# Performance work log

Hardware: AMD Instinct MI355X
Metric: run time of the kernel (lower is better)

## Reference

```python
import jax, jax.numpy as jnp
import numpy as np

INPUT_SIZE = 1024
HIDDEN_SIZE = 1024
BATCH = 8192


def setup_inputs() -> dict:
    key = jax.random.key(0)
    ks = jax.random.split(key, 10)
    s_in = 1.0 / np.sqrt(INPUT_SIZE)
    s_h = 1.0 / np.sqrt(HIDDEN_SIZE)
    return {
        "input": jax.random.normal(ks[0], (BATCH, INPUT_SIZE), jnp.float32),
        "hx": jax.random.normal(ks[1], (BATCH, HIDDEN_SIZE), jnp.float32),
        # weights stored [in, out] (transpose of torch Linear)
        "W_ih": jax.random.uniform(ks[2], (INPUT_SIZE, 2 * HIDDEN_SIZE), jnp.float32, -s_in, s_in),
        "b_ih": jax.random.uniform(ks[3], (2 * HIDDEN_SIZE,), jnp.float32, -s_in, s_in),
        "W_hh": jax.random.uniform(ks[4], (HIDDEN_SIZE, 2 * HIDDEN_SIZE), jnp.float32, -s_h, s_h),
        "b_hh": jax.random.uniform(ks[5], (2 * HIDDEN_SIZE,), jnp.float32, -s_h, s_h),
        "W_c": jax.random.uniform(ks[6], (INPUT_SIZE, HIDDEN_SIZE), jnp.float32, -s_in, s_in),
        "b_c": jax.random.uniform(ks[7], (HIDDEN_SIZE,), jnp.float32, -s_in, s_in),
        "W_hc": jax.random.uniform(ks[8], (HIDDEN_SIZE, HIDDEN_SIZE), jnp.float32, -s_h, s_h),
        "b_hc": jax.random.uniform(ks[9], (HIDDEN_SIZE,), jnp.float32, -s_h, s_h),
    }


def reference(input, hx, W_ih, b_ih, W_hh, b_hh, W_c, b_c, W_hc, b_hc):
    H = hx.shape[1]
    gates = jax.nn.sigmoid(input @ W_ih + b_ih + hx @ W_hh + b_hh)  # [B, 2H]
    z_t, r_t = gates[:, :H], gates[:, H:]
    candidate = jnp.tanh(input @ W_c + b_c + r_t * (hx @ W_hc + b_hc))
    return (1.0 - z_t) * hx + z_t * candidate
```

## Files before the change

### kernel.cpp

```cpp
#include <hip/hip_runtime.h>
#include <hip/hip_bf16.h>
#include <cmath>


typedef __attribute__((ext_vector_type(8))) short bf16x8;
typedef __attribute__((ext_vector_type(4))) float f32x4;
typedef unsigned int u32;

typedef const __attribute__((address_space(1))) u32 gu32;
typedef __attribute__((address_space(3))) u32 su32;

__device__ __forceinline__ unsigned short f2bf(float f) {
  union { float f; u32 u; } v; v.f = f;
  u32 u = v.u;
  u += 0x7FFFu + ((u >> 16) & 1u);
  return (unsigned short)(u >> 16);
}
__device__ __forceinline__ void gload16(void* ldsp, const void* gp) {
  __builtin_amdgcn_global_load_lds((gu32*)gp, (su32*)ldsp, 16, 0, 0);
}
__device__ __forceinline__ float sigmf(float x) { return 1.0f / (1.0f + __expf(-x)); }

__global__ __launch_bounds__(256) void cvt_all(
    const float* __restrict__ In, const float* __restrict__ Hx,
    const float* __restrict__ Wih, const float* __restrict__ Whh,
    const float* __restrict__ Wc,  const float* __restrict__ Whc,
    unsigned short* __restrict__ wsIn, unsigned short* __restrict__ wsHx,
    unsigned short* __restrict__ wsWih, unsigned short* __restrict__ wsWhh,
    unsigned short* __restrict__ wsWc,  unsigned short* __restrict__ wsWhc)
{
  int bid = blockIdx.x;
  if (bid < 8192) {
    int gid = bid * 256 + threadIdx.x;
    const float* src; unsigned short* dst; int idx;
    if (gid < (1 << 20)) { src = In; dst = wsIn; idx = gid; }
    else                 { src = Hx; dst = wsHx; idx = gid - (1 << 20); }
    int m = idx >> 7, t = idx & 127;
    const float4* s = (const float4*)(src + (size_t)m * 1024 + t * 8);
    float4 a = s[0], b = s[1];
    int row = m & 127;
    size_t tile = (size_t)(m >> 7) * 32 + (t >> 2);
    int sw = (t & 3) ^ ((row >> 1) & 3);
    bf16x8 v;
    v[0] = (short)f2bf(a.x); v[1] = (short)f2bf(a.y); v[2] = (short)f2bf(a.z); v[3] = (short)f2bf(a.w);
    v[4] = (short)f2bf(b.x); v[5] = (short)f2bf(b.y); v[6] = (short)f2bf(b.z); v[7] = (short)f2bf(b.w);
    *(bf16x8*)(dst + tile * 4096 + row * 32 + sw * 8) = v;
  } else {
    int wb = bid - 8192;
    const float* W; unsigned short* dst; int NW; int local;
    if (wb < 1024)      { W = Wih; dst = wsWih; NW = 2048; local = wb; }
    else if (wb < 2048) { W = Whh; dst = wsWhh; NW = 2048; local = wb - 1024; }
    else if (wb < 2560) { W = Wc;  dst = wsWc;  NW = 1024; local = wb - 2048; }
    else                { W = Whc; dst = wsWhc; NW = 1024; local = wb - 2560; }
    int nb = local >> 5, kb = local & 31;
    int n  = nb * 64 + (threadIdx.x & 63);
    int k0 = kb * 32 + (threadIdx.x >> 6) * 8;
    bf16x8 v;
    #pragma unroll
    for (int b = 0; b < 8; ++b) v[b] = (short)f2bf(W[(size_t)(k0 + b) * NW + n]);
    int row = n & 63;
    size_t tile = (size_t)(n >> 6) * 32 + (k0 >> 5);
    int sw = ((k0 >> 3) & 3) ^ ((row >> 1) & 3);
    *(bf16x8*)(dst + tile * 2048 + row * 32 + sw * 8) = v;
  }
}

__global__ __launch_bounds__(256, 2) void gru_gemm(
    const unsigned short* __restrict__ ws,
    const float* __restrict__ Hx,
    const float* __restrict__ bih, const float* __restrict__ bhh,
    const float* __restrict__ bc, const float* __restrict__ bhc,
    float* __restrict__ out)
{
  __shared__ unsigned short lds[16384];
  const int tid  = threadIdx.x;
  const int lane = tid & 63;
  const int wave = tid >> 6;
  const int wm = wave >> 1, wn = wave & 1;
  const int bid = blockIdx.x;
  const int i = bid & 63;
  const int j = bid >> 6;
  const int r15 = lane & 15;
  const int q   = lane >> 4;

  const int rw = wn * 32 + r15;
  const u32 vo = (u32)(rw * 32 + ((q ^ ((rw >> 1) & 3)) << 3));
  const unsigned short* Wp0 = ws + 16777216u + (u32)j * 65536u + vo;
  const unsigned short* Wp1 = ws + 16777216u + (u32)(j + 16) * 65536u + vo;
  const unsigned short* Wp2 = ws + 18874368u + (u32)j * 65536u + vo;
  const unsigned short* Wp3 = ws + 18874368u + (u32)(j + 16) * 65536u + vo;
  const unsigned short* Wp4 = ws + 20971520u + (u32)j * 65536u + vo;
  const unsigned short* Wp5 = ws + 22020096u + (u32)j * 65536u + vo;

  const unsigned short* srcA[4];
  #pragma unroll
  for (int c0 = 0; c0 < 4; ++c0) {
    int c = wave * 4 + c0;
    srcA[c0] = (c < 8 ? ws + (size_t)i * 131072 + c * 512
                      : ws + 8388608 + (size_t)i * 131072 + (c - 8) * 512) + lane * 8;
  }
  const int dstA = wave * 4 * 512;

  int aOff[4];
  #pragma unroll
  for (int mr = 0; mr < 4; ++mr) {
    int row = wm * 64 + mr * 16 + r15;
    aOff[mr] = row * 32 + ((q ^ ((row >> 1) & 3)) << 3);
  }

  f32x4 accZ[4][2], accR[4][2], accC[4][2], accH[4][2];
  #pragma unroll
  for (int a = 0; a < 4; ++a)
    #pragma unroll
    for (int b = 0; b < 2; ++b) {
      accZ[a][b] = (f32x4)(0.0f); accR[a][b] = (f32x4)(0.0f);
      accC[a][b] = (f32x4)(0.0f); accH[a][b] = (f32x4)(0.0f);
    }

  auto stage = [&](int bufBase, int s) {
    #pragma unroll
    for (int c0 = 0; c0 < 4; ++c0)
      gload16((void*)&lds[bufBase + dstA + c0 * 512],
              (const void*)(srcA[c0] + (size_t)s * 4096));
  };

  bf16x8 w0a, w0b, w1a, w1b, w2a, w2b, w3a, w3b, w4a, w4b, w5a, w5b;
  #define LOADW(v, P, NR, T) v = *(const bf16x8*)((P) + (u32)(T) * 2048u + (u32)(NR) * 512u)

  #define MFMA_(a,b,c) __builtin_amdgcn_mfma_f32_16x16x32_bf16(a, b, c, 0, 0, 0)

  #define STEP(B, OB, SN, TN, DOSTAGE) {                                         \
    if (DOSTAGE) stage(OB, SN);                                                  \
    bf16x8 aIn[4], aHx[4];                                                       \
    _Pragma("unroll")                                                            \
    for (int mr = 0; mr < 4; ++mr) {                                             \
      aIn[mr] = *(const bf16x8*)&lds[(B) + aOff[mr]];                            \
      aHx[mr] = *(const bf16x8*)&lds[(B) + 4096 + aOff[mr]];                     \
    }                                                                            \
    _Pragma("unroll")                                                            \
    for (int mr = 0; mr < 4; ++mr) {                                             \
      accZ[mr][0] = MFMA_(aIn[mr], w0a, accZ[mr][0]);                            \
      accZ[mr][1] = MFMA_(aIn[mr], w0b, accZ[mr][1]);                            \
      accZ[mr][0] = MFMA_(aHx[mr], w2a, accZ[mr][0]);                            \
      accZ[mr][1] = MFMA_(aHx[mr], w2b, accZ[mr][1]);                            \
    }                                                                            \
    LOADW(w0a, Wp0, 0, TN); LOADW(w0b, Wp0, 1, TN);                              \
    LOADW(w2a, Wp2, 0, TN); LOADW(w2b, Wp2, 1, TN);                              \
    _Pragma("unroll")                                                            \
    for (int mr = 0; mr < 4; ++mr) {                                             \
      accR[mr][0] = MFMA_(aIn[mr], w1a, accR[mr][0]);                            \
      accR[mr][1] = MFMA_(aIn[mr], w1b, accR[mr][1]);                            \
      accR[mr][0] = MFMA_(aHx[mr], w3a, accR[mr][0]);                            \
      accR[mr][1] = MFMA_(aHx[mr], w3b, accR[mr][1]);                            \
    }                                                                            \
    LOADW(w1a, Wp1, 0, TN); LOADW(w1b, Wp1, 1, TN);                              \
    LOADW(w3a, Wp3, 0, TN); LOADW(w3b, Wp3, 1, TN);                              \
    _Pragma("unroll")                                                            \
    for (int mr = 0; mr < 4; ++mr) {                                             \
      accC[mr][0] = MFMA_(aIn[mr], w4a, accC[mr][0]);                            \
      accC[mr][1] = MFMA_(aIn[mr], w4b, accC[mr][1]);                            \
      accH[mr][0] = MFMA_(aHx[mr], w5a, accH[mr][0]);                            \
      accH[mr][1] = MFMA_(aHx[mr], w5b, accH[mr][1]);                            \
    }                                                                            \
    LOADW(w4a, Wp4, 0, TN); LOADW(w4b, Wp4, 1, TN);                              \
    LOADW(w5a, Wp5, 0, TN); LOADW(w5b, Wp5, 1, TN);                              \
    __syncthreads();                       \
  }

  stage(0, 0);
  LOADW(w0a, Wp0, 0, 0); LOADW(w0b, Wp0, 1, 0);
  LOADW(w2a, Wp2, 0, 0); LOADW(w2b, Wp2, 1, 0);
  LOADW(w1a, Wp1, 0, 0); LOADW(w1b, Wp1, 1, 0);
  LOADW(w3a, Wp3, 0, 0); LOADW(w3b, Wp3, 1, 0);
  LOADW(w4a, Wp4, 0, 0); LOADW(w4b, Wp4, 1, 0);
  LOADW(w5a, Wp5, 0, 0); LOADW(w5b, Wp5, 1, 0);
  __syncthreads();

  #pragma unroll 1
  for (int it = 0; it < 16; ++it) {
    const int s = it * 2;
    const int t1 = s + 1;
    const int t2 = s + 2 <= 31 ? s + 2 : 31;
    STEP(0,    8192, t1, t1, true)
    STEP(8192, 0,    t2, t2, it < 15)
  }
  #undef STEP
  #undef LOADW
  #undef MFMA_

  const int n0 = j * 64 + wn * 32;
  const int m0 = i * 128 + wm * 64;
  #pragma unroll
  for (int nr = 0; nr < 2; ++nr) {
    int n = n0 + nr * 16 + r15;
    float bz  = bih[n] + bhh[n];
    float br  = bih[1024 + n] + bhh[1024 + n];
    float bcv = bc[n], bhcv = bhc[n];
    #pragma unroll
    for (int mr = 0; mr < 4; ++mr) {
      #pragma unroll
      for (int v = 0; v < 4; ++v) {
        int m = m0 + mr * 16 + q * 4 + v;
        float z  = sigmf(accZ[mr][nr][v] + bz);
        float rr = sigmf(accR[mr][nr][v] + br);
        float cd = tanhf(accC[mr][nr][v] + bcv + rr * (accH[mr][nr][v] + bhcv));
        float h  = Hx[(size_t)m * 1024 + n];
        out[(size_t)m * 1024 + n] = (1.0f - z) * h + z * cd;
      }
    }
  }
}

__global__ __launch_bounds__(256) void gru_fallback(
    const float* __restrict__ In, const float* __restrict__ Hx,
    const float* __restrict__ Wih, const float* __restrict__ bih,
    const float* __restrict__ Whh, const float* __restrict__ bhh,
    const float* __restrict__ Wc, const float* __restrict__ bc,
    const float* __restrict__ Whc, const float* __restrict__ bhc,
    float* __restrict__ out)
{
  __shared__ float sIn[64][17], sHx[64][17];
  __shared__ float sW[6][16][68];
  const int tid = threadIdx.x;
  const int j = blockIdx.x & 15, i = blockIdx.x >> 4;
  const int tx = tid & 15, ty = tid >> 4;
  float accZ[4][4] = {}, accR[4][4] = {}, accC[4][4] = {}, accH[4][4] = {};
  const int ms = tid >> 2, kq = (tid & 3) * 4;
  const int wk = tid >> 4, wn4 = (tid & 15) * 4;
  for (int k0 = 0; k0 < 1024; k0 += 16) {
    __syncthreads();
    {
      float4 a = *(const float4*)&In[(size_t)(i * 64 + ms) * 1024 + k0 + kq];
      sIn[ms][kq] = a.x; sIn[ms][kq + 1] = a.y; sIn[ms][kq + 2] = a.z; sIn[ms][kq + 3] = a.w;
      float4 b = *(const float4*)&Hx[(size_t)(i * 64 + ms) * 1024 + k0 + kq];
      sHx[ms][kq] = b.x; sHx[ms][kq + 1] = b.y; sHx[ms][kq + 2] = b.z; sHx[ms][kq + 3] = b.w;
    }
    {
      float4 w0 = *(const float4*)&Wih[(size_t)(k0 + wk) * 2048 + j * 64 + wn4];
      float4 w1 = *(const float4*)&Wih[(size_t)(k0 + wk) * 2048 + 1024 + j * 64 + wn4];
      float4 w2 = *(const float4*)&Whh[(size_t)(k0 + wk) * 2048 + j * 64 + wn4];
      float4 w3 = *(const float4*)&Whh[(size_t)(k0 + wk) * 2048 + 1024 + j * 64 + wn4];
      float4 w4 = *(const float4*)&Wc[(size_t)(k0 + wk) * 1024 + j * 64 + wn4];
      float4 w5 = *(const float4*)&Whc[(size_t)(k0 + wk) * 1024 + j * 64 + wn4];
      sW[0][wk][wn4] = w0.x; sW[0][wk][wn4+1] = w0.y; sW[0][wk][wn4+2] = w0.z; sW[0][wk][wn4+3] = w0.w;
      sW[1][wk][wn4] = w1.x; sW[1][wk][wn4+1] = w1.y; sW[1][wk][wn4+2] = w1.z; sW[1][wk][wn4+3] = w1.w;
      sW[2][wk][wn4] = w2.x; sW[2][wk][wn4+1] = w2.y; sW[2][wk][wn4+2] = w2.z; sW[2][wk][wn4+3] = w2.w;
      sW[3][wk][wn4] = w3.x; sW[3][wk][wn4+1] = w3.y; sW[3][wk][wn4+2] = w3.z; sW[3][wk][wn4+3] = w3.w;
      sW[4][wk][wn4] = w4.x; sW[4][wk][wn4+1] = w4.y; sW[4][wk][wn4+2] = w4.z; sW[4][wk][wn4+3] = w4.w;
      sW[5][wk][wn4] = w5.x; sW[5][wk][wn4+1] = w5.y; sW[5][wk][wn4+2] = w5.z; sW[5][wk][wn4+3] = w5.w;
    }
    __syncthreads();
    for (int kk = 0; kk < 16; ++kk) {
      float aI[4], aH[4];
      #pragma unroll
      for (int im = 0; im < 4; ++im) { aI[im] = sIn[ty * 4 + im][kk]; aH[im] = sHx[ty * 4 + im][kk]; }
      #pragma unroll
      for (int jn = 0; jn < 4; ++jn) {
        float w0 = sW[0][kk][tx * 4 + jn], w1 = sW[1][kk][tx * 4 + jn], w2 = sW[2][kk][tx * 4 + jn];
        float w3 = sW[3][kk][tx * 4 + jn], w4 = sW[4][kk][tx * 4 + jn], w5 = sW[5][kk][tx * 4 + jn];
        #pragma unroll
        for (int im = 0; im < 4; ++im) {
          accZ[im][jn] += aI[im] * w0 + aH[im] * w2;
          accR[im][jn] += aI[im] * w1 + aH[im] * w3;
          accC[im][jn] += aI[im] * w4;
          accH[im][jn] += aH[im] * w5;
        }
      }
    }
  }
  #pragma unroll
  for (int jn = 0; jn < 4; ++jn) {
    int n = j * 64 + tx * 4 + jn;
    float bz  = bih[n] + bhh[n];
    float br  = bih[1024 + n] + bhh[1024 + n];
    float bcv = bc[n], bhcv = bhc[n];
    #pragma unroll
    for (int im = 0; im < 4; ++im) {
      int m = i * 64 + ty * 4 + im;
      float z  = sigmf(accZ[im][jn] + bz);
      float rr = sigmf(accR[im][jn] + br);
      float cd = tanhf(accC[im][jn] + bcv + rr * (accH[im][jn] + bhcv));
      float h  = Hx[(size_t)m * 1024 + n];
      out[(size_t)m * 1024 + n] = (1.0f - z) * h + z * cd;
    }
  }
}

extern "C" void kernel_launch(void* const* d_in, const int* in_sizes, int n_in,
                              void* d_out, int out_size, void* d_ws, size_t ws_size,
                              hipStream_t stream) {
  const float* In  = (const float*)d_in[0];
  const float* Hx  = (const float*)d_in[1];
  const float* Wih = (const float*)d_in[2];
  const float* bih = (const float*)d_in[3];
  const float* Whh = (const float*)d_in[4];
  const float* bhh = (const float*)d_in[5];
  const float* Wc  = (const float*)d_in[6];
  const float* bc  = (const float*)d_in[7];
  const float* Whc = (const float*)d_in[8];
  const float* bhc = (const float*)d_in[9];
  float* out = (float*)d_out;

  const size_t WS_NEED = 46137344ull;
  if (ws_size >= WS_NEED) {
    unsigned short* ws    = (unsigned short*)d_ws;
    unsigned short* wsIn  = ws;
    unsigned short* wsHx  = ws + 8388608;
    unsigned short* wsWih = ws + 16777216;
    unsigned short* wsWhh = ws + 18874368;
    unsigned short* wsWc  = ws + 20971520;
    unsigned short* wsWhc = ws + 22020096;
    cvt_all<<<11264, 256, 0, stream>>>(In, Hx, Wih, Whh, Wc, Whc,
                                       wsIn, wsHx, wsWih, wsWhh, wsWc, wsWhc);
    gru_gemm<<<1024, 256, 0, stream>>>(ws, Hx, bih, bhh, bc, bhc, out);
  } else {
    gru_fallback<<<2048, 256, 0, stream>>>(In, Hx, Wih, bih, Whh, bhh, Wc, bc, Whc, bhc, out);
  }
}
```

Baseline: 142.1 us.

## Give each wave private LDS A-tile buffers and drop block barriers

Each wave now stages its own copy of the A (input and hx) K-slices into a private double buffer in LDS, so the per-step __syncthreads is replaced with explicit vmcnt waits. Wave-pair data is loaded twice (waves sharing wm duplicate the loads), LDS use doubles to 64KB per block, and a block-index swizzle groups blocks to improve L2 reuse. This trades extra global/L2 traffic and possibly lower occupancy for removal of barrier stalls. Correctness relies on the hand-counted vmcnt values matching the outstanding load counts.

Result: slower. 151.0 us (+6.3%).

```diff
diff --git a/kernel.cpp b/kernel.cpp
--- a/kernel.cpp
+++ b/kernel.cpp
@@ -72,14 +72,15 @@
     const float* __restrict__ bc, const float* __restrict__ bhc,
     float* __restrict__ out)
 {
-  __shared__ unsigned short lds[16384];
+  __shared__ unsigned short lds[32768];
   const int tid  = threadIdx.x;
   const int lane = tid & 63;
   const int wave = tid >> 6;
   const int wm = wave >> 1, wn = wave & 1;
   const int bid = blockIdx.x;
-  const int i = bid & 63;
-  const int j = bid >> 6;
+  const int swz = (bid & 7) * 128 + (bid >> 3);
+  const int i = swz & 63;
+  const int j = swz >> 6;
   const int r15 = lane & 15;
   const int q   = lane >> 4;
 
@@ -92,20 +93,19 @@
   const unsigned short* Wp4 = ws + 20971520u + (u32)j * 65536u + vo;
   const unsigned short* Wp5 = ws + 22020096u + (u32)j * 65536u + vo;
 
-  const unsigned short* srcA[4];
-  #pragma unroll
-  for (int c0 = 0; c0 < 4; ++c0) {
-    int c = wave * 4 + c0;
-    srcA[c0] = (c < 8 ? ws + (size_t)i * 131072 + c * 512
-                      : ws + 8388608 + (size_t)i * 131072 + (c - 8) * 512) + lane * 8;
-  }
-  const int dstA = wave * 4 * 512;
+  const unsigned short* srcA[8];
+  #pragma unroll
+  for (int c = 0; c < 4; ++c) {
+    srcA[c]     = ws +            (size_t)i * 131072 + (wm * 4 + c) * 512 + lane * 8;
+    srcA[4 + c] = ws + 8388608u + (size_t)i * 131072 + (wm * 4 + c) * 512 + lane * 8;
+  }
+  const int wbase = wave * 8192;
 
   int aOff[4];
   #pragma unroll
   for (int mr = 0; mr < 4; ++mr) {
-    int row = wm * 64 + mr * 16 + r15;
-    aOff[mr] = row * 32 + ((q ^ ((row >> 1) & 3)) << 3);
+    int r = mr * 16 + r15;
+    aOff[mr] = r * 32 + ((q ^ ((r >> 1) & 3)) << 3);
   }
 
   f32x4 accZ[4][2], accR[4][2], accC[4][2], accH[4][2];
@@ -119,23 +119,22 @@
 
   auto stage = [&](int bufBase, int s) {
     #pragma unroll
-    for (int c0 = 0; c0 < 4; ++c0)
-      gload16((void*)&lds[bufBase + dstA + c0 * 512],
-              (const void*)(srcA[c0] + (size_t)s * 4096));
+    for (int c = 0; c < 8; ++c)
+      gload16((void*)&lds[bufBase + c * 512],
+              (const void*)(srcA[c] + (size_t)s * 4096));
   };
 
   bf16x8 w0a, w0b, w1a, w1b, w2a, w2b, w3a, w3b, w4a, w4b, w5a, w5b;
   #define LOADW(v, P, NR, T) v = *(const bf16x8*)((P) + (u32)(T) * 2048u + (u32)(NR) * 512u)
-
   #define MFMA_(a,b,c) __builtin_amdgcn_mfma_f32_16x16x32_bf16(a, b, c, 0, 0, 0)
 
-  #define STEP(B, OB, SN, TN, DOSTAGE) {                                         \
-    if (DOSTAGE) stage(OB, SN);                                                  \
+  #define STEP(BUF, TN, SD, DOSTAGE) {                                           \
+    asm volatile("s_waitcnt vmcnt(32)" ::: "memory");                            \
     bf16x8 aIn[4], aHx[4];                                                       \
     _Pragma("unroll")                                                            \
     for (int mr = 0; mr < 4; ++mr) {                                             \
-      aIn[mr] = *(const bf16x8*)&lds[(B) + aOff[mr]];                            \
-      aHx[mr] = *(const bf16x8*)&lds[(B) + 4096 + aOff[mr]];                     \
+      aIn[mr] = *(const bf16x8*)&lds[(BUF) + aOff[mr]];                          \
+      aHx[mr] = *(const bf16x8*)&lds[(BUF) + 2048 + aOff[mr]];                   \
     }                                                                            \
     _Pragma("unroll")                                                            \
     for (int mr = 0; mr < 4; ++mr) {                                             \
@@ -144,6 +143,7 @@
       accZ[mr][0] = MFMA_(aHx[mr], w2a, accZ[mr][0]);                            \
       accZ[mr][1] = MFMA_(aHx[mr], w2b, accZ[mr][1]);                            \
     }                                                                            \
+    if (DOSTAGE) stage(BUF, SD);                                                 \
     LOADW(w0a, Wp0, 0, TN); LOADW(w0b, Wp0, 1, TN);                              \
     LOADW(w2a, Wp2, 0, TN); LOADW(w2b, Wp2, 1, TN);                              \
     _Pragma("unroll")                                                            \
@@ -164,25 +164,25 @@
     }                                                                            \
     LOADW(w4a, Wp4, 0, TN); LOADW(w4b, Wp4, 1, TN);                              \
     LOADW(w5a, Wp5, 0, TN); LOADW(w5b, Wp5, 1, TN);                              \
-    __syncthreads();                       \
-  }
-
-  stage(0, 0);
+  }
+
+  stage(wbase, 0);
+  stage(wbase + 4096, 1);
   LOADW(w0a, Wp0, 0, 0); LOADW(w0b, Wp0, 1, 0);
   LOADW(w2a, Wp2, 0, 0); LOADW(w2b, Wp2, 1, 0);
   LOADW(w1a, Wp1, 0, 0); LOADW(w1b, Wp1, 1, 0);
   LOADW(w3a, Wp3, 0, 0); LOADW(w3b, Wp3, 1, 0);
   LOADW(w4a, Wp4, 0, 0); LOADW(w4b, Wp4, 1, 0);
   LOADW(w5a, Wp5, 0, 0); LOADW(w5b, Wp5, 1, 0);
-  __syncthreads();
+  asm volatile("s_waitcnt vmcnt(20)" ::: "memory");
 
   #pragma unroll 1
   for (int it = 0; it < 16; ++it) {
-    const int s = it * 2;
-    const int t1 = s + 1;
-    const int t2 = s + 2 <= 31 ? s + 2 : 31;
-    STEP(0,    8192, t1, t1, true)
-    STEP(8192, 0,    t2, t2, it < 15)
+    const int s = 2 * it;
+    const int tn1 = s + 1;
+    const int tn2 = s + 2 <= 31 ? s + 2 : 31;
+    STEP(wbase,        tn1, s + 2, it < 15)
+    STEP(wbase + 4096, tn2, s + 3, it < 15)
   }
   #undef STEP
   #undef LOADW
```
